# Performance work log

Hardware: AMD Instinct MI355X
Metric: run time of the kernel (lower is better)

The kernel has to match this reference:

```python
import jax, jax.numpy as jnp
import numpy as np

N_ATOMS = 100000; E_ATOMS = 200000; N_AMINO = 10240; E_AMINO = 20480; B = 512
D_IN = 40; D_E = 11; H1 = 20; H2 = 20; H3 = 20; D_AA = 8; H_ARMA = 128; K = 3; T = 7
F1 = 256; F2 = 128; F3 = 64


def setup_inputs() -> dict:
    key = jax.random.key(0)
    ks = jax.random.split(key, 40)
    s = 0.05
    inp = {}
    inp['x'] = jax.random.normal(ks[0], (N_ATOMS, D_IN), dtype=jnp.float32)
    inp['edge_index'] = jax.random.randint(ks[1], (2, E_ATOMS), 0, N_ATOMS, dtype=jnp.int32)
    inp['edge_attr'] = jax.random.normal(ks[2], (E_ATOMS, D_E), dtype=jnp.float32)
    inp['monomer_labels'] = jax.random.randint(ks[3], (N_ATOMS,), 0, N_AMINO, dtype=jnp.int32)
    inp['aminoacids_features'] = jax.random.normal(ks[4], (N_AMINO, D_AA), dtype=jnp.float32)
    inp['amino_edge_index'] = jax.random.randint(ks[5], (2, E_AMINO), 0, N_AMINO, dtype=jnp.int32)
    inp['amino_batch'] = jnp.sort(jax.random.randint(ks[6], (N_AMINO,), 0, B, dtype=jnp.int32))
    # NNConv params: edge-MLP (Linear(D_E, in*out)), root weight, bias
    inp['nn1_w'] = jax.random.normal(ks[7], (D_E, D_IN * H1)) * s
    inp['nn1_b'] = jax.random.normal(ks[8], (D_IN * H1,)) * s
    inp['root1'] = jax.random.normal(ks[9], (D_IN, H1)) * s
    inp['b1'] = jax.random.normal(ks[10], (H1,)) * s
    inp['nn2_w'] = jax.random.normal(ks[11], (D_E, H1 * H2)) * s
    inp['nn2_b'] = jax.random.normal(ks[12], (H1 * H2,)) * s
    inp['root2'] = jax.random.normal(ks[13], (H1, H2)) * s
    inp['b2'] = jax.random.normal(ks[14], (H2,)) * s
    inp['nn3_w'] = jax.random.normal(ks[15], (D_E, H2 * H3)) * s
    inp['nn3_b'] = jax.random.normal(ks[16], (H2 * H3,)) * s
    inp['root3'] = jax.random.normal(ks[17], (H2, H3)) * s
    inp['b3'] = jax.random.normal(ks[18], (H3,)) * s
    # ARMAConv params (K stacks, T layers, shared_weights=False)
    F_ARMA_IN = H3 + D_AA
    inp['arma_init'] = jax.random.normal(ks[19], (K, F_ARMA_IN, H_ARMA)) * s
    inp['arma_w'] = jax.random.normal(ks[20], (T - 1, K, H_ARMA, H_ARMA)) * s
    inp['arma_root'] = jax.random.normal(ks[21], (T, K, F_ARMA_IN, H_ARMA)) * s
    inp['arma_bias'] = jax.random.normal(ks[22], (T, K, 1, H_ARMA)) * s
    # FCN head
    inp['l1_w'] = jax.random.normal(ks[23], (H_ARMA, F1)) * s
    inp['l1_b'] = jax.random.normal(ks[24], (F1,)) * s
    inp['l2_w'] = jax.random.normal(ks[25], (F1, F2)) * s
    inp['l2_b'] = jax.random.normal(ks[26], (F2,)) * s
    inp['l3_w'] = jax.random.normal(ks[27], (F2, F3)) * s
    inp['l3_b'] = jax.random.normal(ks[28], (F3,)) * s
    inp['l4_w'] = jax.random.normal(ks[29], (F3, 1)) * s
    inp['l4_b'] = jax.random.normal(ks[30], (1,)) * s
    return inp


def _nnconv(x, ei, ea, w_nn, b_nn, root, bias, out_dim):
    # PyG NNConv (aggr='add'): out_i = x_i @ root + sum_{j->i} x_j @ W(e_ji) + bias
    E, d_in = ea.shape[0], x.shape[1]
    W = (ea @ w_nn + b_nn).reshape(E, d_in, out_dim)  # per-edge weight matrices
    msg = jnp.einsum('ei,eio->eo', x[ei[0]], W)       # gather + batched matvec
    agg = jax.ops.segment_sum(msg, ei[1], num_segments=x.shape[0])
    return x @ root + agg + bias


def _arma(x, ei, init_w, w, root_w, bias):
    # PyG ARMAConv: sym-normalized adjacency (no self loops), K stacks, T layers, ReLU act
    N = x.shape[0]
    deg = jax.ops.segment_sum(jnp.ones(ei.shape[1], x.dtype), ei[1], num_segments=N)
    dinv = jnp.where(deg > 0, deg ** -0.5, 0.0)
    norm = dinv[ei[0]] * dinv[ei[1]]  # [E_amino]
    out = None
    for t in range(T):
        h = jnp.einsum('nf,kfo->kno', x, init_w) if t == 0 else jnp.einsum('knf,kfo->kno', out, w[t - 1])
        msg = h[:, ei[0], :] * norm[None, :, None]
        h = jax.vmap(lambda m: jax.ops.segment_sum(m, ei[1], num_segments=N))(msg)
        h = h + jnp.einsum('nf,kfo->kno', x, root_w[t]) + bias[t]
        out = jax.nn.relu(h)
    return out.mean(0)  # mean over stacks


def reference(x, edge_index, edge_attr, monomer_labels, aminoacids_features,
              amino_edge_index, amino_batch,
              nn1_w, nn1_b, root1, b1, nn2_w, nn2_b, root2, b2, nn3_w, nn3_b, root3, b3,
              arma_init, arma_w, arma_root, arma_bias,
              l1_w, l1_b, l2_w, l2_b, l3_w, l3_b, l4_w, l4_b):
    h = jax.nn.relu(_nnconv(x, edge_index, edge_attr, nn1_w, nn1_b, root1, b1, H1))
    h = jax.nn.relu(_nnconv(h, edge_index, edge_attr, nn2_w, nn2_b, root2, b2, H2))
    h = jax.nn.relu(_nnconv(h, edge_index, edge_attr, nn3_w, nn3_b, root3, b3, H3))
    # per-graph loop flattened: atoms -> amino-acid sum readout (graphs disjoint)
    aa = jax.ops.segment_sum(h, monomer_labels, num_segments=N_AMINO)
    aa = jnp.concatenate([aa, aminoacids_features], axis=1)  # [N_AMINO, H3+8]
    aa = jax.nn.relu(_arma(aa, amino_edge_index, arma_init, arma_w, arma_root, arma_bias))
    g = jax.ops.segment_sum(aa, amino_batch, num_segments=B)  # per-graph sum readout
    p = jax.nn.relu(g @ l1_w + l1_b)  # dropout is identity in eval mode
    p = jax.nn.relu(p @ l2_w + l2_b)
    p = jax.nn.relu(p @ l3_w + l3_b)
    return (p @ l4_w + l4_b).reshape(-1)
```

## Files before the change

kernel.cpp:

```cpp
#include <hip/hip_runtime.h>

#define N_ATOMS 100000
#define E_ATOMS 200000
#define N_AMINO 10240
#define E_AMINO 20480
#define NGRAPH 512
#define DIN0 40
#define D_E 11
#define HD 20
#define D_AA 8
#define HA 128
#define KS 3
#define TL 7
#define F1 256
#define F2 128
#define F3 64
#define NTILE 16
#define ECAP 64
#define EAW 12

typedef unsigned short u16;
typedef unsigned int u32;
typedef __attribute__((ext_vector_type(8))) short short8;
typedef __attribute__((ext_vector_type(4))) float f32x4;

__device__ __forceinline__ float b2f(u16 u) {
    union { u32 i; float f; } v; v.i = ((u32)u) << 16; return v.f;
}
__device__ __forceinline__ u16 f2b(float f) {
    union { float f; u32 i; } v; v.f = f;
    u32 x = v.i;
    return (u16)((x + (((x >> 16) & 1u) + 0x7fffu)) >> 16);
}

__global__ __launch_bounds__(256) void k_prep0(
    const float* __restrict__ w1, const float* __restrict__ b1,
    const float* __restrict__ w2, const float* __restrict__ b2,
    const float* __restrict__ w3, const float* __restrict__ b3,
    float* __restrict__ M1, float* __restrict__ M2, float* __restrict__ M3,
    const float* __restrict__ af, float* __restrict__ aa,
    int* __restrict__ cs, int* __restrict__ cd,
    int* __restrict__ ca, int* __restrict__ cl) {
    int t = blockIdx.x * 256 + threadIdx.x;
    if (t < 9600) {
        int i = t / 240, c = t % 240;
        M1[t] = (c < 220) ? w1[(c / 20) * 800 + i * 20 + (c % 20)] : b1[i * 20 + (c - 220)];
    } else if (t < 14400) {
        int tt = t - 9600, i = tt / 240, c = tt % 240;
        M2[tt] = (c < 220) ? w2[(c / 20) * 400 + i * 20 + (c % 20)] : b2[i * 20 + (c - 220)];
    } else if (t < 19200) {
        int tt = t - 14400, i = tt / 240, c = tt % 240;
        M3[tt] = (c < 220) ? w3[(c / 20) * 400 + i * 20 + (c % 20)] : b3[i * 20 + (c - 220)];
    } else if (t < 19200 + N_AMINO * D_AA) {
        int idx = t - 19200, m = idx / D_AA, j = idx % D_AA;
        aa[m * 28 + HD + j] = af[idx];
    } else {
        int z = t - 19200 - N_AMINO * D_AA;
        if (z < N_ATOMS) cs[z] = 0;
        else if (z < 2 * N_ATOMS) cd[z - N_ATOMS] = 0;
        else if (z < 2 * N_ATOMS + N_AMINO) ca[z - 2 * N_ATOMS] = 0;
        else if (z < 2 * N_ATOMS + 2 * N_AMINO) cl[z - 2 * N_ATOMS - N_AMINO] = 0;
    }
}
#define PREP0_N (19200 + N_AMINO * D_AA + 2 * N_ATOMS + 2 * N_AMINO)

#define WP0_ELEMS (KS * 8192)
#define WP1_ELEMS (6 * KS * 20480)
__global__ __launch_bounds__(256) void k_cvtwp2(
    const float* __restrict__ ai, const float* __restrict__ aw,
    const float* __restrict__ arw, u16* __restrict__ Wp) {
    int g = blockIdx.x * 256 + threadIdx.x;
    if (g < WP0_ELEMS) {
        int k = g / 8192, r = g % 8192;
        int kb = r >> 12, rem = r & 4095;
        int c = rem >> 5, qj = rem & 31;
        int krow = kb * 32 + qj;
        float v = 0.f;
        if (krow < 28)      v = ai[((size_t)k * 28 + krow) * HA + c];
        else if (krow < 56) v = arw[((size_t)k * 28 + (krow - 28)) * HA + c];
        Wp[g] = f2b(v);
    } else if (g < WP0_ELEMS + WP1_ELEMS) {
        int gg = g - WP0_ELEMS;
        int mat = gg / 20480, r = gg % 20480;
        int kb = r / 4096, rem = r & 4095;
        int c = rem >> 5, qj = rem & 31;
        int krow = kb * 32 + qj;
        int tm1 = mat / KS, k = mat % KS;
        float v = 0.f;
        if (krow < 128)      v = aw[((size_t)mat * 128 + krow) * HA + c];
        else if (krow < 156) v = arw[(((size_t)(tm1 + 1) * KS + k) * 28 + (krow - 128)) * HA + c];
        Wp[g] = f2b(v);
    }
}

#define NBS 98
#define NBA 10

__global__ __launch_bounds__(256) void k_csr_count(
    const int* __restrict__ esrc, const int* __restrict__ edst,
    const int* __restrict__ adst, const int* __restrict__ lbl,
    int* __restrict__ cs, int* __restrict__ cd,
    int* __restrict__ ca, int* __restrict__ cl) {
    int t = blockIdx.x * 256 + threadIdx.x;
    if (t < E_ATOMS) atomicAdd(cs + esrc[t], 1);
    else if (t < 2 * E_ATOMS) atomicAdd(cd + edst[t - E_ATOMS], 1);
    else if (t < 2 * E_ATOMS + E_AMINO) atomicAdd(ca + adst[t - 2 * E_ATOMS], 1);
    else if (t < 2 * E_ATOMS + E_AMINO + N_ATOMS) atomicAdd(cl + lbl[t - 2 * E_ATOMS - E_AMINO], 1);
}
__device__ __forceinline__ void seg_decode(int bx, int* blk, int* n, int* which) {
    if (bx < NBS)            { *which = 0; *blk = bx;             *n = N_ATOMS; }
    else if (bx < 2 * NBS)   { *which = 1; *blk = bx - NBS;       *n = N_ATOMS; }
    else if (bx < 2 * NBS + NBA) { *which = 2; *blk = bx - 2 * NBS; *n = N_AMINO; }
    else                     { *which = 3; *blk = bx - 2 * NBS - NBA; *n = N_AMINO; }
}
__global__ __launch_bounds__(256) void k_scan1(
    const int* __restrict__ cs, int* __restrict__ soff,
    const int* __restrict__ cd, int* __restrict__ doff,
    const int* __restrict__ ca, int* __restrict__ aoff,
    const int* __restrict__ cl, int* __restrict__ loff,
    int* __restrict__ bsum) {
    int blk, n, which;
    seg_decode(blockIdx.x, &blk, &n, &which);
    const int* c = which == 0 ? cs : which == 1 ? cd : which == 2 ? ca : cl;
    int* o = which == 0 ? soff : which == 1 ? doff : which == 2 ? aoff : loff;
    int tx = threadIdx.x, lane = tx & 63, w = tx >> 6;
    int i0 = blk * 1024 + tx * 4;
    int v[4];
#pragma unroll
    for (int q = 0; q < 4; ++q) v[q] = (i0 + q < n) ? c[i0 + q] : 0;
    int s = v[0] + v[1] + v[2] + v[3];
    int inc = s;
#pragma unroll
    for (int d = 1; d < 64; d <<= 1) {
        int u = __shfl_up(inc, d, 64);
        if (lane >= d) inc += u;
    }
    __shared__ int wsum[4];
    if (lane == 63) wsum[w] = inc;
    __syncthreads();
    int wo = 0;
    for (int i = 0; i < w; ++i) wo += wsum[i];
    int run = wo + inc - s;
#pragma unroll
    for (int q = 0; q < 4; ++q) {
        if (i0 + q < n) o[i0 + q] = run;
        run += v[q];
    }
    if (tx == 255) bsum[blockIdx.x] = wo + inc;
}
__global__ __launch_bounds__(128) void k_scan2(
    int* __restrict__ bsum, int* __restrict__ soff, int* __restrict__ doff,
    int* __restrict__ aoff, int* __restrict__ loff) {
    int bx = blockIdx.x;
    int nb   = (bx < 2) ? NBS : NBA;
    int base = (bx == 0) ? 0 : (bx == 1) ? NBS : (bx == 2) ? 2 * NBS : 2 * NBS + NBA;
    int* b = bsum + base;
    int tx = threadIdx.x, lane = tx & 63;
    int v = (tx < nb) ? b[tx] : 0;
    int inc = v;
#pragma unroll
    for (int d = 1; d < 64; d <<= 1) {
        int u = __shfl_up(inc, d, 64);
        if (lane >= d) inc += u;
    }
    __shared__ int w0;
    if (tx == 63) w0 = inc;
    __syncthreads();
    int excl = inc - v + ((tx >= 64) ? w0 : 0);
    if (tx < nb) b[tx] = excl;
    if (tx == nb - 1) {
        int tot = excl + v;
        if (bx == 0) soff[N_ATOMS] = tot;
        else if (bx == 1) doff[N_ATOMS] = tot;
        else if (bx == 2) aoff[N_AMINO] = tot;
        else loff[N_AMINO] = tot;
    }
}
__global__ __launch_bounds__(256) void k_scan3(
    int* __restrict__ soff, int* __restrict__ doff,
    int* __restrict__ aoff, int* __restrict__ loff,
    const int* __restrict__ bsum,
    int* __restrict__ us, int* __restrict__ ud,
    int* __restrict__ ua, int* __restrict__ ul) {
    int blk, n, which;
    seg_decode(blockIdx.x, &blk, &n, &which);
    int* o = which == 0 ? soff : which == 1 ? doff : which == 2 ? aoff : loff;
    int* cu = which == 0 ? us : which == 1 ? ud : which == 2 ? ua : ul;
    int add = bsum[blockIdx.x];
    int i0 = blk * 1024 + threadIdx.x * 4;
#pragma unroll
    for (int q = 0; q < 4; ++q)
        if (i0 + q < n) { int val = o[i0 + q] + add; o[i0 + q] = val; cu[i0 + q] = val; }
}
__global__ __launch_bounds__(256) void k_csr_fill(
    const int* __restrict__ esrc, const int* __restrict__ edst,
    const float* __restrict__ ea,
    int* __restrict__ us, int* __restrict__ srcP, u16* __restrict__ eaP,
    int* __restrict__ ud, int* __restrict__ dslot,
    const int* __restrict__ aei, int* __restrict__ ua, int* __restrict__ aeid,
    const int* __restrict__ aoff, float* __restrict__ nrm,
    const int* __restrict__ lbl, int* __restrict__ ul, int* __restrict__ lnid) {
    int t = blockIdx.x * 256 + threadIdx.x;
    if (t < E_ATOMS) {
        int jj = atomicAdd(us + esrc[t], 1);
        srcP[jj] = esrc[t];
        const float* e0 = ea + (size_t)t * D_E;
        u16* e1 = eaP + (size_t)jj * EAW;
#pragma unroll
        for (int k = 0; k < D_E; ++k) e1[k] = f2b(e0[k]);
        e1[D_E] = f2b(1.0f);
        int p = atomicAdd(ud + edst[t], 1);
        dslot[p] = jj;
    } else if (t < E_ATOMS + E_AMINO) {
        int e = t - E_ATOMS;
        int p = atomicAdd(ua + aei[E_AMINO + e], 1);
        aeid[p] = e;
    } else if (t < E_ATOMS + 2 * E_AMINO) {
        int e = t - E_ATOMS - E_AMINO;
        int s = aei[e], d = aei[E_AMINO + e];
        int ds = aoff[s + 1] - aoff[s], dd = aoff[d + 1] - aoff[d];
        float a = ds > 0 ? rsqrtf((float)ds) : 0.f;
        float b = dd > 0 ? rsqrtf((float)dd) : 0.f;
        nrm[e] = a * b;
    } else if (t < E_ATOMS + 2 * E_AMINO + N_ATOMS) {
        int n = t - E_ATOMS - 2 * E_AMINO;
        int p = atomicAdd(ul + lbl[n], 1);
        lnid[p] = n;
    }
}

template <int DIN, bool RAW>
__global__ __launch_bounds__(256, 6) void nnconv_edge9(
    const void* __restrict__ xin, const u16* __restrict__ eaP,
    const int* __restrict__ srcP, const int* __restrict__ soff,
    const float* __restrict__ Mg, u16* __restrict__ msg) {
    __shared__ __align__(16) float y3[NTILE * 240];
    __shared__ __align__(16) float xs[NTILE * DIN];
    __shared__ __align__(16) float eaS[ECAP * 12];
    __shared__ int srcS[ECAP];
    int tx = threadIdx.x;
    int n0 = blockIdx.x * NTILE;
    int j0 = soff[n0], j1 = soff[n0 + NTILE];
    for (int i = tx; i < NTILE * DIN; i += 256)
        xs[i] = RAW ? ((const float*)xin)[(size_t)n0 * DIN + i]
                    : b2f(((const u16*)xin)[(size_t)n0 * DIN + i]);
    {
        int cn0 = j1 - j0; if (cn0 > ECAP) cn0 = ECAP;
        for (int i = tx; i < cn0; i += 256) srcS[i] = srcP[j0 + i] - n0;
        const u32* eg = (const u32*)(eaP + (size_t)j0 * EAW);
        for (int i = tx; i < cn0 * 6; i += 256) {
            u32 pv = eg[i];
            eaS[2 * i]     = b2f((u16)(pv & 0xffff));
            eaS[2 * i + 1] = b2f((u16)(pv >> 16));
        }
    }
    __syncthreads();
    if (tx < 240) {
        float m[DIN];
#pragma unroll
        for (int i = 0; i < DIN; ++i) m[i] = Mg[i * 240 + tx];
        int st = (tx < 220) ? (tx % 20) * 12 + tx / 20 : (tx - 220) * 12 + 11;
        const float4* xs4 = (const float4*)xs;
        for (int nl = 0; nl < NTILE; nl += 4) {
            const float4* x0 = xs4 + nl * (DIN / 4);
            float a0 = 0.f, a1 = 0.f, a2 = 0.f, a3 = 0.f;
#pragma unroll
            for (int ii = 0; ii < DIN / 4; ++ii) {
                float4 v0 = x0[ii];
                float4 v1 = x0[(DIN / 4) + ii];
                float4 v2 = x0[2 * (DIN / 4) + ii];
                float4 v3 = x0[3 * (DIN / 4) + ii];
                float m0 = m[4 * ii], m1 = m[4 * ii + 1], m2 = m[4 * ii + 2], m3 = m[4 * ii + 3];
                a0 += v0.x * m0 + v0.y * m1 + v0.z * m2 + v0.w * m3;
                a1 += v1.x * m0 + v1.y * m1 + v1.z * m2 + v1.w * m3;
                a2 += v2.x * m0 + v2.y * m1 + v2.z * m2 + v2.w * m3;
                a3 += v3.x * m0 + v3.y * m1 + v3.z * m2 + v3.w * m3;
            }
            y3[(nl + 0) * 240 + st] = a0;
            y3[(nl + 1) * 240 + st] = a1;
            y3[(nl + 2) * 240 + st] = a2;
            y3[(nl + 3) * 240 + st] = a3;
        }
    }
    __syncthreads();
    int c0 = j0;
    while (true) {
        int cn = j1 - c0; if (cn > ECAP) cn = ECAP;
        for (int p = tx; p < cn * 20; p += 256) {
            int e = p / 20, o = p - e * 20;
            const float4* ev = (const float4*)&eaS[e * 12];
            const float4* yr = (const float4*)&y3[srcS[e] * 240 + o * 12];
            float4 e0 = ev[0], e1 = ev[1], e2 = ev[2];
            float4 q0 = yr[0], q1 = yr[1], q2 = yr[2];
            float mv = e0.x * q0.x + e0.y * q0.y + e0.z * q0.z + e0.w * q0.w
                     + e1.x * q1.x + e1.y * q1.y + e1.z * q1.z + e1.w * q1.w
                     + e2.x * q2.x + e2.y * q2.y + e2.z * q2.z + e2.w * q2.w;
            msg[(size_t)(c0 + e) * 20 + o] = f2b(mv);
        }
        c0 += cn;
        if (c0 >= j1) break;
        __syncthreads();
        int cm = j1 - c0; if (cm > ECAP) cm = ECAP;
        for (int i = tx; i < cm; i += 256) srcS[i] = srcP[c0 + i] - n0;
        const u32* eg = (const u32*)(eaP + (size_t)c0 * EAW);
        for (int i = tx; i < cm * 6; i += 256) {
            u32 pv = eg[i];
            eaS[2 * i]     = b2f((u16)(pv & 0xffff));
            eaS[2 * i + 1] = b2f((u16)(pv >> 16));
        }
        __syncthreads();
    }
}

template <int DIN, bool RAW>
__global__ __launch_bounds__(256) void nnconv_reduce(
    const void* __restrict__ xin, const float* __restrict__ root,
    const float* __restrict__ bias, const int* __restrict__ doff,
    const int* __restrict__ dslot, const u16* __restrict__ msg,
    u16* __restrict__ hout) {
    __shared__ float Rl[DIN * HD + HD];
    for (int t = threadIdx.x; t < DIN * HD; t += 256) Rl[t] = root[t];
    if (threadIdx.x < HD) Rl[DIN * HD + threadIdx.x] = bias[threadIdx.x];
    __syncthreads();
    int t = blockIdx.x * 256 + threadIdx.x;
    if (t >= N_ATOMS * HD) return;
    int n = t / HD, o = t % HD;
    float acc = Rl[DIN * HD + o];
    int j1 = doff[n + 1];
    for (int j = doff[n]; j < j1; ++j)
        acc += b2f(msg[(size_t)dslot[j] * 20 + o]);
    const float* xf = (const float*)xin + (size_t)n * DIN;
    const u16*   xb = (const u16*)xin + (size_t)n * DIN;
#pragma unroll
    for (int i = 0; i < DIN; ++i)
        acc += (RAW ? xf[i] : b2f(xb[i])) * Rl[i * HD + o];
    hout[t] = f2b(fmaxf(acc, 0.f));
}

__global__ __launch_bounds__(256) void aa_gather(
    const u16* __restrict__ h3, const int* __restrict__ loff,
    const int* __restrict__ lnid, float* __restrict__ aa) {
    int t = blockIdx.x * 256 + threadIdx.x;
    if (t >= N_AMINO * HD) return;
    int m = t / HD, o = t % HD;
    float s = 0.f;
    int j1 = loff[m + 1];
    for (int j = loff[m]; j < j1; ++j)
        s += b2f(h3[(size_t)lnid[j] * HD + o]);
    aa[m * 28 + o] = s;
}

__global__ __launch_bounds__(256) void k_gaa(
    const float* __restrict__ aa, const int* __restrict__ aoff,
    const int* __restrict__ aeid, const int* __restrict__ aei,
    const float* __restrict__ nrm, u16* __restrict__ A0) {
    int t = blockIdx.x * 256 + threadIdx.x;
    if (t >= N_AMINO * 64) return;
    int n = t >> 6, c = t & 63;
    float v = 0.f;
    if (c < 28) {
        int j1 = aoff[n + 1];
        for (int jj = aoff[n]; jj < j1; ++jj) {
            int e = aeid[jj], s = aei[e];
            v += nrm[e] * aa[(size_t)s * 28 + c];
        }
    } else if (c < 56) {
        v = aa[(size_t)n * 28 + (c - 28)];
    }
    A0[t] = f2b(v);
}

__global__ __launch_bounds__(256) void arma_l0(
    const u16* __restrict__ A0, const u16* __restrict__ Wp0,
    const float* __restrict__ abi, u16* __restrict__ O, size_t kstride) {
    int wave = threadIdx.x >> 6, lane = threadIdx.x & 63;
    int k = blockIdx.y;
    const u16* W = Wp0 + (size_t)k * 8192;
    u16* Ok = O + (size_t)k * kstride;
    const float* bk = abi + (size_t)k * HA;
    int n0 = (blockIdx.x * 4 + wave) * 16;
    int m = lane & 15, q = lane >> 4;
    short8 aF[2];
#pragma unroll
    for (int kb = 0; kb < 2; ++kb)
        aF[kb] = *(const short8*)(A0 + (size_t)(n0 + m) * 64 + kb * 32 + q * 8);
#pragma unroll
    for (int ct = 0; ct < 8; ++ct) {
        int c0 = ct * 16;
        float b = bk[c0 + m];
        f32x4 acc = {b, b, b, b};
#pragma unroll
        for (int kb = 0; kb < 2; ++kb) {
            short8 bF = *(const short8*)(W + (size_t)((kb * 128 + c0 + m) * 32 + q * 8));
            acc = __builtin_amdgcn_mfma_f32_16x16x32_bf16(aF[kb], bF, acc, 0, 0, 0);
        }
#pragma unroll
        for (int r = 0; r < 4; ++r)
            Ok[(size_t)(n0 + q * 4 + r) * HA + c0 + m] = f2b(fmaxf(acc[r], 0.f));
    }
}

__global__ __launch_bounds__(256) void arma_lt(
    const u16* __restrict__ Oprev, const u16* __restrict__ Wm,
    const float* __restrict__ abit, const float* __restrict__ aa,
    const int* __restrict__ aoff, const int* __restrict__ aeid,
    const int* __restrict__ aei, const float* __restrict__ nrm,
    u16* __restrict__ Onext, size_t kstride) {
    __shared__ __align__(16) u16 As[64 * 160];
    int tx = threadIdx.x;
    int k = blockIdx.y;
    int n0b = blockIdx.x * 64;
    const u16* Op = Oprev + (size_t)k * kstride;
    const u16* W  = Wm + (size_t)k * 20480;
    for (int i = tx; i < 1024; i += 256) {
        int nl = i >> 4, cb = i & 15;
        int n = n0b + nl;
        int j1 = aoff[n + 1];
        float a0 = 0.f, a1 = 0.f, a2 = 0.f, a3 = 0.f;
        float a4 = 0.f, a5 = 0.f, a6 = 0.f, a7 = 0.f;
        for (int jj = aoff[n]; jj < j1; ++jj) {
            int e = aeid[jj], s = aei[e];
            float nm = nrm[e];
            uint4 hv = *(const uint4*)(Op + (size_t)s * HA + cb * 8);
            a0 += nm * b2f((u16)(hv.x & 0xffff));
            a1 += nm * b2f((u16)(hv.x >> 16));
            a2 += nm * b2f((u16)(hv.y & 0xffff));
            a3 += nm * b2f((u16)(hv.y >> 16));
            a4 += nm * b2f((u16)(hv.z & 0xffff));
            a5 += nm * b2f((u16)(hv.z >> 16));
            a6 += nm * b2f((u16)(hv.w & 0xffff));
            a7 += nm * b2f((u16)(hv.w >> 16));
        }
        uint4 pk;
        pk.x = (u32)f2b(a0) | ((u32)f2b(a1) << 16);
        pk.y = (u32)f2b(a2) | ((u32)f2b(a3) << 16);
        pk.z = (u32)f2b(a4) | ((u32)f2b(a5) << 16);
        pk.w = (u32)f2b(a6) | ((u32)f2b(a7) << 16);
        *(uint4*)&As[nl * 160 + cb * 8] = pk;
    }
    {
        int nl = tx >> 2, cb = tx & 3;
        int n = n0b + nl;
        float av[8];
#pragma unroll
        for (int j = 0; j < 8; ++j) {
            int c = cb * 8 + j;
            av[j] = (c < 28) ? aa[(size_t)n * 28 + c] : 0.f;
        }
        uint4 pk;
        pk.x = (u32)f2b(av[0]) | ((u32)f2b(av[1]) << 16);
        pk.y = (u32)f2b(av[2]) | ((u32)f2b(av[3]) << 16);
        pk.z = (u32)f2b(av[4]) | ((u32)f2b(av[5]) << 16);
        pk.w = (u32)f2b(av[6]) | ((u32)f2b(av[7]) << 16);
        *(uint4*)&As[nl * 160 + 128 + cb * 8] = pk;
    }
    __syncthreads();
    int wave = tx >> 6, lane = tx & 63;
    int m = lane & 15, q = lane >> 4;
    int wl = wave * 16 + m;
    short8 aF[5];
#pragma unroll
    for (int kb = 0; kb < 5; ++kb)
        aF[kb] = *(const short8*)&As[wl * 160 + kb * 32 + q * 8];
    int n0 = n0b + wave * 16;
    u16* On = Onext + (size_t)k * kstride;
    const float* bk = abit + (size_t)k * HA;
#pragma unroll
    for (int ct = 0; ct < 8; ++ct) {
        int c0 = ct * 16;
        float b = bk[c0 + m];
        f32x4 acc = {b, b, b, b};
#pragma unroll
        for (int kb = 0; kb < 5; ++kb) {
            short8 bF = *(const short8*)(W + (size_t)((kb * 128 + c0 + m) * 32 + q * 8));
            acc = __builtin_amdgcn_mfma_f32_16x16x32_bf16(aF[kb], bF, acc, 0, 0, 0);
        }
#pragma unroll
        for (int r = 0; r < 4; ++r)
            On[(size_t)(n0 + q * 4 + r) * HA + c0 + m] = f2b(fmaxf(acc[r], 0.f));
    }
}

__global__ __launch_bounds__(256) void head2(
    const u16* __restrict__ O, size_t kstride, const int* __restrict__ bat,
    const float* __restrict__ l1w, const float* __restrict__ l1b,
    const float* __restrict__ l2w, const float* __restrict__ l2b,
    const float* __restrict__ l3w, const float* __restrict__ l3b,
    const float* __restrict__ l4w, const float* __restrict__ l4b,
    float* __restrict__ outp) {
    __shared__ float sg[HA], sp1[F1], sp2[F2], sp3[F3];
    int b = blockIdx.x, tx = threadIdx.x;
    int lo = 0, hi = N_AMINO;
    while (lo < hi) { int mid = (lo + hi) >> 1; if (bat[mid] < b) lo = mid + 1; else hi = mid; }
    int s = lo;
    lo = 0; hi = N_AMINO;
    while (lo < hi) { int mid = (lo + hi) >> 1; if (bat[mid] < b + 1) lo = mid + 1; else hi = mid; }
    int e = lo;
    if (tx < HA) {
        float acc = 0.f;
        for (int n = s; n < e; ++n)
            acc += b2f(O[(size_t)n * HA + tx]) + b2f(O[kstride + (size_t)n * HA + tx])
                 + b2f(O[2 * kstride + (size_t)n * HA + tx]);
        sg[tx] = acc * (1.f / 3.f);
    }
    __syncthreads();
    {   float acc = l1b[tx];
        for (int f = 0; f < HA; ++f) acc += sg[f] * l1w[f * F1 + tx];
        sp1[tx] = fmaxf(acc, 0.f); }
    __syncthreads();
    if (tx < F2) {
        float acc = l2b[tx];
        for (int f = 0; f < F1; ++f) acc += sp1[f] * l2w[f * F2 + tx];
        sp2[tx] = fmaxf(acc, 0.f); }
    __syncthreads();
    if (tx < F3) {
        float acc = l3b[tx];
        for (int f = 0; f < F2; ++f) acc += sp2[f] * l3w[f * F3 + tx];
        sp3[tx] = fmaxf(acc, 0.f); }
    __syncthreads();
    if (tx < 64) {
        float p = sp3[tx] * l4w[tx];
        for (int off = 32; off > 0; off >>= 1) p += __shfl_down(p, off, 64);
        if (tx == 0) outp[b] = p + l4b[0];
    }
}

#define OFF_M1    ((size_t)0)
#define OFF_M2    ((size_t)38400)
#define OFF_M3    ((size_t)57600)
#define OFF_AOFF  ((size_t)76800)
#define OFF_AEID  ((size_t)118016)
#define OFF_NRM   ((size_t)199936)
#define OFF_AA    ((size_t)281856)
#define OFF_HA    ((size_t)2891008)
#define OFF_HB    ((size_t)6891008)
#define OFF_MSG   ((size_t)10891008)
#define OFF_SOFF  ((size_t)18891008)
#define OFF_DOFF  ((size_t)19291136)
#define OFF_DSLOT ((size_t)19691264)
#define OFF_LOFF  ((size_t)20491264)
#define OFF_LNID  ((size_t)20532480)
#define OFF_CS    ((size_t)20932480)
#define OFF_CD    ((size_t)21332480)
#define OFF_CA    ((size_t)21732480)
#define OFF_CL    ((size_t)21773440)
#define OFF_US    ((size_t)21814400)
#define OFF_UD    ((size_t)22214400)
#define OFF_UA    ((size_t)22614400)
#define OFF_UL    ((size_t)22655360)
#define OFF_BSUM  ((size_t)22696320)
#define OFF_EAP   ((size_t)22697216)
#define OFF_SRCP  ((size_t)27497216)
#define OFF_WP    ((size_t)28297216)
#define OFF_OB    ((size_t)2891008)
#define OFF_A0    ((size_t)10891008)
#define OFF_OA    ((size_t)18619648)

extern "C" void kernel_launch(void* const* d_in, const int* in_sizes, int n_in,
                              void* d_out, int out_size, void* d_ws, size_t ws_size,
                              hipStream_t stream) {
    (void)in_sizes; (void)n_in; (void)out_size; (void)ws_size;
    const float* x   = (const float*)d_in[0];
    const int*   ei  = (const int*)d_in[1];
    const float* ea  = (const float*)d_in[2];
    const int*   lbl = (const int*)d_in[3];
    const float* af  = (const float*)d_in[4];
    const int*   aei = (const int*)d_in[5];
    const int*   bat = (const int*)d_in[6];
    const float* nn1w = (const float*)d_in[7];  const float* nn1b = (const float*)d_in[8];
    const float* rt1  = (const float*)d_in[9];  const float* b1   = (const float*)d_in[10];
    const float* nn2w = (const float*)d_in[11]; const float* nn2b = (const float*)d_in[12];
    const float* rt2  = (const float*)d_in[13]; const float* b2   = (const float*)d_in[14];
    const float* nn3w = (const float*)d_in[15]; const float* nn3b = (const float*)d_in[16];
    const float* rt3  = (const float*)d_in[17]; const float* b3   = (const float*)d_in[18];
    const float* ai   = (const float*)d_in[19]; const float* aw   = (const float*)d_in[20];
    const float* arw  = (const float*)d_in[21]; const float* abi  = (const float*)d_in[22];
    const float* l1w  = (const float*)d_in[23]; const float* l1b  = (const float*)d_in[24];
    const float* l2w  = (const float*)d_in[25]; const float* l2b  = (const float*)d_in[26];
    const float* l3w  = (const float*)d_in[27]; const float* l3b  = (const float*)d_in[28];
    const float* l4w  = (const float*)d_in[29]; const float* l4b  = (const float*)d_in[30];
    float* outp = (float*)d_out;

    char* ws = (char*)d_ws;
    float* M1    = (float*)(ws + OFF_M1);
    float* M2    = (float*)(ws + OFF_M2);
    float* M3    = (float*)(ws + OFF_M3);
    int*   aoff  = (int*)(ws + OFF_AOFF);
    int*   aeid  = (int*)(ws + OFF_AEID);
    float* nrm   = (float*)(ws + OFF_NRM);
    float* aa    = (float*)(ws + OFF_AA);
    u16*   hA    = (u16*)(ws + OFF_HA);
    u16*   hB    = (u16*)(ws + OFF_HB);
    u16*   msg   = (u16*)(ws + OFF_MSG);
    int*   soff  = (int*)(ws + OFF_SOFF);
    int*   doff  = (int*)(ws + OFF_DOFF);
    int*   dslot = (int*)(ws + OFF_DSLOT);
    int*   loff  = (int*)(ws + OFF_LOFF);
    int*   lnid  = (int*)(ws + OFF_LNID);
    int*   cs    = (int*)(ws + OFF_CS);
    int*   cd    = (int*)(ws + OFF_CD);
    int*   ca    = (int*)(ws + OFF_CA);
    int*   cl    = (int*)(ws + OFF_CL);
    int*   us    = (int*)(ws + OFF_US);
    int*   ud    = (int*)(ws + OFF_UD);
    int*   ua    = (int*)(ws + OFF_UA);
    int*   ul    = (int*)(ws + OFF_UL);
    int*   bsum  = (int*)(ws + OFF_BSUM);
    u16*   eaP   = (u16*)(ws + OFF_EAP);
    int*   srcP  = (int*)(ws + OFF_SRCP);
    u16*   Wp    = (u16*)(ws + OFF_WP);
    u16*   A0    = (u16*)(ws + OFF_A0);
    u16*   OA    = (u16*)(ws + OFF_OA);
    u16*   OB    = (u16*)(ws + OFF_OB);

    const int* esrc = ei;
    const int* edst = ei + E_ATOMS;
    const int* adst = aei + E_AMINO;

    k_prep0<<<(PREP0_N + 255) / 256, 256, 0, stream>>>(
        nn1w, nn1b, nn2w, nn2b, nn3w, nn3b, M1, M2, M3, af, aa, cs, cd, ca, cl);
    k_cvtwp2<<<(WP0_ELEMS + WP1_ELEMS + 255) / 256, 256, 0, stream>>>(ai, aw, arw, Wp);
    k_csr_count<<<(2 * E_ATOMS + E_AMINO + N_ATOMS + 255) / 256, 256, 0, stream>>>(
        esrc, edst, adst, lbl, cs, cd, ca, cl);
    k_scan1<<<2 * NBS + 2 * NBA, 256, 0, stream>>>(cs, soff, cd, doff, ca, aoff, cl, loff, bsum);
    k_scan2<<<4, 128, 0, stream>>>(bsum, soff, doff, aoff, loff);
    k_scan3<<<2 * NBS + 2 * NBA, 256, 0, stream>>>(soff, doff, aoff, loff, bsum, us, ud, ua, ul);
    k_csr_fill<<<(E_ATOMS + 2 * E_AMINO + N_ATOMS + 255) / 256, 256, 0, stream>>>(
        esrc, edst, ea, us, srcP, eaP, ud, dslot, aei, ua, aeid, aoff, nrm, lbl, ul, lnid);

    const int GT = N_ATOMS / NTILE;
    const int GF = (N_ATOMS * HD + 255) / 256;
    nnconv_edge9<DIN0, true ><<<GT, 256, 0, stream>>>(x,  eaP, srcP, soff, M1, msg);
    nnconv_reduce<DIN0, true ><<<GF, 256, 0, stream>>>(x,  rt1, b1, doff, dslot, msg, hA);
    nnconv_edge9<HD,   false><<<GT, 256, 0, stream>>>(hA, eaP, srcP, soff, M2, msg);
    nnconv_reduce<HD,   false><<<GF, 256, 0, stream>>>(hA, rt2, b2, doff, dslot, msg, hB);
    nnconv_edge9<HD,   false><<<GT, 256, 0, stream>>>(hB, eaP, srcP, soff, M3, msg);
    nnconv_reduce<HD,   false><<<GF, 256, 0, stream>>>(hB, rt3, b3, doff, dslot, msg, hA);
    aa_gather<<<(N_AMINO * HD + 255) / 256, 256, 0, stream>>>(hA, loff, lnid, aa);

    const size_t KH = (size_t)N_AMINO * HA;
    k_gaa<<<(N_AMINO * 64 + 255) / 256, 256, 0, stream>>>(aa, aoff, aeid, aei, nrm, A0);
    arma_l0<<<dim3(160, KS), 256, 0, stream>>>(A0, Wp, abi, OA, KH);
    for (int t = 1; t < TL; ++t) {
        const u16* Oin  = (t & 1) ? OA : OB;
        u16*       Oout = (t & 1) ? OB : OA;
        arma_lt<<<dim3(160, KS), 256, 0, stream>>>(
            Oin, Wp + WP0_ELEMS + (size_t)((t - 1) * KS) * 20480,
            abi + (size_t)t * KS * HA, aa, aoff, aeid, aei, nrm, Oout, KH);
    }
    head2<<<NGRAPH, 256, 0, stream>>>(OA, KH, bat, l1w, l1b, l2w, l2b,
                                      l3w, l3b, l4w, l4b, outp);
}
```

Before: 542.3 us.

## Use bf16 MFMA for per-node edge-weight projection in NNConv edge kernel

Replaces the scalar fp32 FMA loop that computes each node tile's projection onto the 240-column edge-MLP weight with 16x16x32 bf16 MFMA instructions. The weight matrices are pre-packed into bf16 K-blocked layouts padded to 32 rows, and node features are staged in shared memory as padded bf16 instead of fp32. This cuts VALU work and register pressure in the edge kernel. In exchange, the first layer's fp32 input and all weights are rounded to bf16 and the K dimension carries zero padding.

```diff
diff --git a/kernel.cpp b/kernel.cpp
--- a/kernel.cpp
+++ b/kernel.cpp
@@ -33,36 +33,54 @@
     return (u16)((x + (((x >> 16) & 1u) + 0x7fffu)) >> 16);
 }
 
+#define MB1_ELEMS 15360
+#define MB2_ELEMS 7680
+#define PREP0_N (MB1_ELEMS + 2 * MB2_ELEMS + N_AMINO * D_AA + 2 * N_ATOMS + 2 * N_AMINO)
 __global__ __launch_bounds__(256) void k_prep0(
     const float* __restrict__ w1, const float* __restrict__ b1,
     const float* __restrict__ w2, const float* __restrict__ b2,
     const float* __restrict__ w3, const float* __restrict__ b3,
-    float* __restrict__ M1, float* __restrict__ M2, float* __restrict__ M3,
+    u16* __restrict__ Mb1, u16* __restrict__ Mb2, u16* __restrict__ Mb3,
     const float* __restrict__ af, float* __restrict__ aa,
     int* __restrict__ cs, int* __restrict__ cd,
     int* __restrict__ ca, int* __restrict__ cl) {
     int t = blockIdx.x * 256 + threadIdx.x;
-    if (t < 9600) {
-        int i = t / 240, c = t % 240;
-        M1[t] = (c < 220) ? w1[(c / 20) * 800 + i * 20 + (c % 20)] : b1[i * 20 + (c - 220)];
-    } else if (t < 14400) {
-        int tt = t - 9600, i = tt / 240, c = tt % 240;
-        M2[tt] = (c < 220) ? w2[(c / 20) * 400 + i * 20 + (c % 20)] : b2[i * 20 + (c - 220)];
-    } else if (t < 19200) {
-        int tt = t - 14400, i = tt / 240, c = tt % 240;
-        M3[tt] = (c < 220) ? w3[(c / 20) * 400 + i * 20 + (c % 20)] : b3[i * 20 + (c - 220)];
-    } else if (t < 19200 + N_AMINO * D_AA) {
-        int idx = t - 19200, m = idx / D_AA, j = idx % D_AA;
+    if (t < MB1_ELEMS) {
+        int kb = t / 7680, rem = t % 7680;
+        int c = rem >> 5, qj = rem & 31;
+        int krow = kb * 32 + qj;
+        float v = 0.f;
+        if (krow < DIN0)
+            v = (c < 220) ? w1[(c / 20) * 800 + krow * 20 + (c % 20)]
+                          : b1[krow * 20 + (c - 220)];
+        Mb1[t] = f2b(v);
+    } else if (t < MB1_ELEMS + MB2_ELEMS) {
+        int tt = t - MB1_ELEMS;
+        int c = tt >> 5, qj = tt & 31;
+        float v = 0.f;
+        if (qj < HD)
+            v = (c < 220) ? w2[(c / 20) * 400 + qj * 20 + (c % 20)]
+                          : b2[qj * 20 + (c - 220)];
+        Mb2[tt] = f2b(v);
+    } else if (t < MB1_ELEMS + 2 * MB2_ELEMS) {
+        int tt = t - MB1_ELEMS - MB2_ELEMS;
+        int c = tt >> 5, qj = tt & 31;
+        float v = 0.f;
+        if (qj < HD)
+            v = (c < 220) ? w3[(c / 20) * 400 + qj * 20 + (c % 20)]
+                          : b3[qj * 20 + (c - 220)];
+        Mb3[tt] = f2b(v);
+    } else if (t < MB1_ELEMS + 2 * MB2_ELEMS + N_AMINO * D_AA) {
+        int idx = t - MB1_ELEMS - 2 * MB2_ELEMS, m = idx / D_AA, j = idx % D_AA;
         aa[m * 28 + HD + j] = af[idx];
     } else {
-        int z = t - 19200 - N_AMINO * D_AA;
+        int z = t - MB1_ELEMS - 2 * MB2_ELEMS - N_AMINO * D_AA;
         if (z < N_ATOMS) cs[z] = 0;
         else if (z < 2 * N_ATOMS) cd[z - N_ATOMS] = 0;
         else if (z < 2 * N_ATOMS + N_AMINO) ca[z - 2 * N_ATOMS] = 0;
         else if (z < 2 * N_ATOMS + 2 * N_AMINO) cl[z - 2 * N_ATOMS - N_AMINO] = 0;
     }
 }
-#define PREP0_N (19200 + N_AMINO * D_AA + 2 * N_ATOMS + 2 * N_AMINO)
 
 #define WP0_ELEMS (KS * 8192)
 #define WP1_ELEMS (6 * KS * 20480)
@@ -229,21 +247,27 @@
     }
 }
 
-template <int DIN, bool RAW>
-__global__ __launch_bounds__(256, 6) void nnconv_edge9(
+template <int DIN, int KB, bool RAW>
+__global__ __launch_bounds__(256, 6) void nnconv_edge10(
     const void* __restrict__ xin, const u16* __restrict__ eaP,
     const int* __restrict__ srcP, const int* __restrict__ soff,
-    const float* __restrict__ Mg, u16* __restrict__ msg) {
+    const u16* __restrict__ Mb, u16* __restrict__ msg) {
+    constexpr int KPAD = KB * 32;
     __shared__ __align__(16) float y3[NTILE * 240];
-    __shared__ __align__(16) float xs[NTILE * DIN];
+    __shared__ __align__(16) u16 As[NTILE * KPAD];
     __shared__ __align__(16) float eaS[ECAP * 12];
     __shared__ int srcS[ECAP];
     int tx = threadIdx.x;
     int n0 = blockIdx.x * NTILE;
     int j0 = soff[n0], j1 = soff[n0 + NTILE];
-    for (int i = tx; i < NTILE * DIN; i += 256)
-        xs[i] = RAW ? ((const float*)xin)[(size_t)n0 * DIN + i]
-                    : b2f(((const u16*)xin)[(size_t)n0 * DIN + i]);
+    for (int i = tx; i < NTILE * KPAD; i += 256) {
+        int node = i / KPAD, k = i % KPAD;
+        u16 v = 0;
+        if (k < DIN)
+            v = RAW ? f2b(((const float*)xin)[(size_t)(n0 + node) * DIN + k])
+                    : ((const u16*)xin)[(size_t)(n0 + node) * DIN + k];
+        As[i] = v;
+    }
     {
         int cn0 = j1 - j0; if (cn0 > ECAP) cn0 = ECAP;
         for (int i = tx; i < cn0; i += 256) srcS[i] = srcP[j0 + i] - n0;
@@ -255,31 +279,26 @@
         }
     }
     __syncthreads();
-    if (tx < 240) {
-        float m[DIN];
-#pragma unroll
-        for (int i = 0; i < DIN; ++i) m[i] = Mg[i * 240 + tx];
-        int st = (tx < 220) ? (tx % 20) * 12 + tx / 20 : (tx - 220) * 12 + 11;
-        const float4* xs4 = (const float4*)xs;
-        for (int nl = 0; nl < NTILE; nl += 4) {
-            const float4* x0 = xs4 + nl * (DIN / 4);
-            float a0 = 0.f, a1 = 0.f, a2 = 0.f, a3 = 0.f;
-#pragma unroll
-            for (int ii = 0; ii < DIN / 4; ++ii) {
-                float4 v0 = x0[ii];
-                float4 v1 = x0[(DIN / 4) + ii];
-                float4 v2 = x0[2 * (DIN / 4) + ii];
-                float4 v3 = x0[3 * (DIN / 4) + ii];
-                float m0 = m[4 * ii], m1 = m[4 * ii + 1], m2 = m[4 * ii + 2], m3 = m[4 * ii + 3];
-                a0 += v0.x * m0 + v0.y * m1 + v0.z * m2 + v0.w * m3;
-                a1 += v1.x * m0 + v1.y * m1 + v1.z * m2 + v1.w * m3;
-                a2 += v2.x * m0 + v2.y * m1 + v2.z * m2 + v2.w * m3;
-                a3 += v3.x * m0 + v3.y * m1 + v3.z * m2 + v3.w * m3;
+    {
+        int wave = tx >> 6, lane = tx & 63;
+        int m = lane & 15, q = lane >> 4;
+        short8 aF[KB];
+#pragma unroll
+        for (int kb = 0; kb < KB; ++kb)
+            aF[kb] = *(const short8*)&As[m * KPAD + kb * 32 + q * 8];
+        for (int ct = wave; ct < 15; ct += 4) {
+            int c0 = ct * 16;
+            f32x4 acc = {0.f, 0.f, 0.f, 0.f};
+#pragma unroll
+            for (int kb = 0; kb < KB; ++kb) {
+                short8 bF = *(const short8*)(Mb + (size_t)kb * 7680 + (size_t)(c0 + m) * 32 + q * 8);
+                acc = __builtin_amdgcn_mfma_f32_16x16x32_bf16(aF[kb], bF, acc, 0, 0, 0);
             }
-            y3[(nl + 0) * 240 + st] = a0;
-            y3[(nl + 1) * 240 + st] = a1;
-            y3[(nl + 2) * 240 + st] = a2;
-            y3[(nl + 3) * 240 + st] = a3;
+            int c = c0 + m;
+            int slot = (c < 220) ? (c % 20) * 12 + c / 20 : (c - 220) * 12 + 11;
+#pragma unroll
+            for (int r = 0; r < 4; ++r)
+                y3[(q * 4 + r) * 240 + slot] = acc[r];
         }
     }
     __syncthreads();
@@ -582,9 +601,9 @@
     float* outp = (float*)d_out;
 
     char* ws = (char*)d_ws;
-    float* M1    = (float*)(ws + OFF_M1);
-    float* M2    = (float*)(ws + OFF_M2);
-    float* M3    = (float*)(ws + OFF_M3);
+    u16*   Mb1   = (u16*)(ws + OFF_M1);
+    u16*   Mb2   = (u16*)(ws + OFF_M2);
+    u16*   Mb3   = (u16*)(ws + OFF_M3);
     int*   aoff  = (int*)(ws + OFF_AOFF);
     int*   aeid  = (int*)(ws + OFF_AEID);
     float* nrm   = (float*)(ws + OFF_NRM);
@@ -618,7 +637,7 @@
     const int* adst = aei + E_AMINO;
 
     k_prep0<<<(PREP0_N + 255) / 256, 256, 0, stream>>>(
-        nn1w, nn1b, nn2w, nn2b, nn3w, nn3b, M1, M2, M3, af, aa, cs, cd, ca, cl);
+        nn1w, nn1b, nn2w, nn2b, nn3w, nn3b, Mb1, Mb2, Mb3, af, aa, cs, cd, ca, cl);
     k_cvtwp2<<<(WP0_ELEMS + WP1_ELEMS + 255) / 256, 256, 0, stream>>>(ai, aw, arw, Wp);
     k_csr_count<<<(2 * E_ATOMS + E_AMINO + N_ATOMS + 255) / 256, 256, 0, stream>>>(
         esrc, edst, adst, lbl, cs, cd, ca, cl);
@@ -630,11 +649,11 @@
 
     const int GT = N_ATOMS / NTILE;
     const int GF = (N_ATOMS * HD + 255) / 256;
-    nnconv_edge9<DIN0, true ><<<GT, 256, 0, stream>>>(x,  eaP, srcP, soff, M1, msg);
+    nnconv_edge10<DIN0, 2, true ><<<GT, 256, 0, stream>>>(x,  eaP, srcP, soff, Mb1, msg);
     nnconv_reduce<DIN0, true ><<<GF, 256, 0, stream>>>(x,  rt1, b1, doff, dslot, msg, hA);
-    nnconv_edge9<HD,   false><<<GT, 256, 0, stream>>>(hA, eaP, srcP, soff, M2, msg);
+    nnconv_edge10<HD,   1, false><<<GT, 256, 0, stream>>>(hA, eaP, srcP, soff, Mb2, msg);
     nnconv_reduce<HD,   false><<<GF, 256, 0, stream>>>(hA, rt2, b2, doff, dslot, msg, hB);
-    nnconv_edge9<HD,   false><<<GT, 256, 0, stream>>>(hB, eaP, srcP, soff, M3, msg);
+    nnconv_edge10<HD,   1, false><<<GT, 256, 0, stream>>>(hB, eaP, srcP, soff, Mb3, msg);
     nnconv_reduce<HD,   false><<<GF, 256, 0, stream>>>(hB, rt3, b3, doff, dslot, msg, hA);
     aa_gather<<<(N_AMINO * HD + 255) / 256, 256, 0, stream>>>(hA, loff, lnid, aa);
 
```

Result: faster. 506.4 us (-6.6%).
